# Kernel optimization log

Measured on AMD Instinct MI355X. Metric: run time of the kernel, lower is better.

## Reference

```python
import jax, jax.numpy as jnp
import numpy as np

USER_NUM = 100_000
ITEM_NUM = 50_000
N = USER_NUM + ITEM_NUM          # total nodes in the bipartite graph
HIDDEN = 64
LAYERS = 3
BATCH = 4096
NNZ = 4_800_000                  # ~avg degree 32


def setup_inputs() -> dict:
    key = jax.random.key(0)
    ks = jax.random.split(key, 7)
    emb = jax.random.normal(ks[0], (N, HIDDEN), dtype=jnp.float32) * 0.02
    rows = jax.random.randint(ks[1], (NNZ,), 0, N, dtype=jnp.int32)
    cols = jax.random.randint(ks[2], (NNZ,), 0, N, dtype=jnp.int32)
    # normalized-laplacian-like positive values, scaled ~ 1/avg_degree
    vals = jax.random.uniform(ks[3], (NNZ,), dtype=jnp.float32) * (1.0 / 32.0)
    user = jax.random.randint(ks[4], (BATCH,), 0, USER_NUM, dtype=jnp.int32)
    pos = jax.random.randint(ks[5], (BATCH,), USER_NUM, N, dtype=jnp.int32)
    neg = jax.random.randint(ks[6], (BATCH,), USER_NUM, N, dtype=jnp.int32)
    return {"emb": emb, "vals": vals, "rows": rows, "cols": cols,
            "user": user, "pos": pos, "neg": neg}


def _spmm(rows, cols, vals, x):
    # sparse [N,N] @ dense [N,d] in COO form: gather + scale + segment-sum
    return jax.ops.segment_sum(vals[:, None] * x[cols], rows, num_segments=N)


def reference(emb, vals, rows, cols, user, pos, neg):
    # layer-0 gathers
    user_acc = emb[user]
    pos_acc = emb[pos]
    neg_acc = emb[neg]
    e = emb
    for _ in range(LAYERS):
        e = _spmm(rows, cols, vals, e)
        user_acc = user_acc + e[user]
        pos_acc = pos_acc + e[pos]
        neg_acc = neg_acc + e[neg]
    denom = jnp.float32(LAYERS + 1)
    u = user_acc / denom   # mean over stacked layers
    p = pos_acc / denom
    n = neg_acc / denom
    pos_logits = jnp.einsum('id,id->i', u, p)
    neg_logits = jnp.einsum('id,id->i', u, n)
    # -log(sigmoid(x)) == -log_sigmoid(x) (numerically stable)
    loss = -jax.nn.log_sigmoid(pos_logits - neg_logits)
    return loss.sum()
```

## Files before the change

### kernel.cpp

```cpp
#include <hip/hip_runtime.h>

#define HIDDEN 64
#define PAD 96
#define CHUNK 16384
#define NBMAX 1024
#define E_CAP 9600

typedef unsigned int uint;

__device__ __forceinline__ ushort f2bf(float f) {
    uint u = __float_as_uint(f);
    u = (u + 0x7FFFu + ((u >> 16) & 1u)) >> 16;
    return (ushort)u;
}
__device__ __forceinline__ float bf2f(ushort h) {
    return __uint_as_float(((uint)h) << 16);
}


__global__ void __launch_bounds__(256) k_f2bf(const float4* __restrict__ src,
                                              ushort* __restrict__ dst, int n4) {
    int i = blockIdx.x * blockDim.x + threadIdx.x;
    if (i >= n4) return;
    float4 f = src[i];
    ushort4 o;
    o.x = f2bf(f.x); o.y = f2bf(f.y); o.z = f2bf(f.z); o.w = f2bf(f.w);
    ((ushort4*)dst)[i] = o;
}


__global__ void __launch_bounds__(1024) k_count(const int* __restrict__ rows,
                                                int* __restrict__ partial,
                                                int nnz, int nb) {
    __shared__ int h[NBMAX];
    int t = threadIdx.x;
    for (int i = t; i < nb; i += 1024) h[i] = 0;
    __syncthreads();
    int cb = blockIdx.x * CHUNK;
    #pragma unroll
    for (int j = 0; j < CHUNK / 1024; ++j) {
        int idx = cb + j * 1024 + t;
        if (idx < nnz) atomicAdd(&h[rows[idx] >> 8], 1);
    }
    __syncthreads();
    for (int i = t; i < nb; i += 1024) partial[(size_t)blockIdx.x * nb + i] = h[i];
}

__global__ void __launch_bounds__(1024) k_colscan(const int* __restrict__ partial,
                                                  int* __restrict__ blockoff,
                                                  int* __restrict__ stagecnt,
                                                  int nblk, int nb) {
    __shared__ int s[1024];
    int k = blockIdx.x;
    int t = threadIdx.x;
    int v = (t < nblk) ? partial[(size_t)t * nb + k] : 0;
    s[t] = v;
    __syncthreads();
    for (int d = 1; d < 1024; d <<= 1) {
        int p = (t >= d) ? s[t - d] : 0;
        __syncthreads();
        s[t] += p;
        __syncthreads();
    }
    if (t < nblk) blockoff[(size_t)t * nb + k] = s[t] - v;
    if (t == 1023) stagecnt[k] = s[1023];
}

__global__ void __launch_bounds__(1024) k_bucketscan(const int* __restrict__ stagecnt,
                                                     int* __restrict__ base, int nb) {
    __shared__ int s[1024];
    int t = threadIdx.x;
    int v = (t < nb) ? stagecnt[t] : 0;
    s[t] = v;
    __syncthreads();
    for (int d = 1; d < 1024; d <<= 1) {
        int p = (t >= d) ? s[t - d] : 0;
        __syncthreads();
        s[t] += p;
        __syncthreads();
    }
    if (t < nb) base[t] = s[t] - v;
}

__global__ void __launch_bounds__(1024) k_stage(const int* __restrict__ rows,
                                                const int* __restrict__ cols,
                                                const float* __restrict__ vals,
                                                const int* __restrict__ blockoff,
                                                const int* __restrict__ base,
                                                int2* __restrict__ staged,
                                                int nnz, int nb) {
    __shared__ int cur[NBMAX];
    int t = threadIdx.x;
    for (int i = t; i < nb; i += 1024)
        cur[i] = base[i] + blockoff[(size_t)blockIdx.x * nb + i];
    __syncthreads();
    int cb = blockIdx.x * CHUNK;
    #pragma unroll
    for (int j = 0; j < CHUNK / 1024; ++j) {
        int idx = cb + j * 1024 + t;
        if (idx < nnz) {
            int r = rows[idx];
            int k = r >> 8;
            int slot = atomicAdd(&cur[k], 1);
            staged[slot] = make_int2(cols[idx] | ((r & 255) << 18),
                                     __float_as_int(vals[idx]));
        }
    }
}

__global__ void __launch_bounds__(1024) k_fine(const int2* __restrict__ staged,
                                               const int* __restrict__ base,
                                               const int* __restrict__ stagecnt,
                                               int2* __restrict__ pack,
                                               int* __restrict__ cnt, int n) {
    __shared__ int2 out[E_CAP];
    __shared__ int hist[256], rstart[256], cursor[256], s2[256];
    int k = blockIdx.x;
    int t = threadIdx.x;
    int s0 = base[k];
    int ck = stagecnt[k];
    if (t < 256) hist[t] = 0;
    __syncthreads();
    for (int i = t; i < ck; i += 1024)
        atomicAdd(&hist[((uint)staged[s0 + i].x) >> 18], 1);
    __syncthreads();
    if (t < 256) s2[t] = hist[t];
    __syncthreads();
    for (int d = 1; d < 256; d <<= 1) {
        int p = (t < 256 && t >= d) ? s2[t - d] : 0;
        __syncthreads();
        if (t < 256) s2[t] += p;
        __syncthreads();
    }
    if (t < 256) {
        int rs = s2[t] - hist[t];
        rstart[t] = rs;
        cursor[t] = rs;
        int row = (k << 8) + t;
        if (row < n) cnt[row] = hist[t];
    }
    __syncthreads();
    for (int i = t; i < ck; i += 1024) {
        int2 e = staged[s0 + i];
        int lr = ((uint)e.x) >> 18;
        int slot = atomicAdd(&cursor[lr], 1);
        if (slot < E_CAP) out[slot] = make_int2(e.x & 0x3FFFF, e.y);
    }
    __syncthreads();
    for (int idx = t; idx < 256 * PAD; idx += 1024) {
        int lr = idx / PAD, j = idx - lr * PAD;
        if (j < hist[lr]) {
            int row = (k << 8) + lr;
            pack[(size_t)row * PAD + j] = out[rstart[lr] + j];
        }
    }
}


__device__ __forceinline__ float4 spmm_row4(const int* __restrict__ cnt,
                                            const int2* __restrict__ pack,
                                            const ushort* __restrict__ x,
                                            int row, int lane) {
    int len = cnt[row]; if (len > PAD) len = PAD;
    const int2* base = pack + (size_t)row * PAD;
    int g = (lane & 15) * 4;
    int e = lane >> 4;
    float a0 = 0.f, a1 = 0.f, a2 = 0.f, a3 = 0.f;
    float b0 = 0.f, b1 = 0.f, b2 = 0.f, b3 = 0.f;
    for (int j0 = 0; j0 < len; j0 += 64) {
        int m = len - j0; if (m > 64) m = 64;
        int c = 0; float v = 0.f;
        if (lane < m) {
            int2 cv = base[j0 + lane];
            c = cv.x;
            v = __int_as_float(cv.y);
        }
        int steps = (m + 3) >> 2;
        int s = 0;
        for (; s + 1 < steps; s += 2) {
            int   i0 = 4 * s + e,  i1 = 4 * s + 4 + e;
            int   c0 = __shfl(c, i0); float v0 = __shfl(v, i0);
            int   c1 = __shfl(c, i1); float v1 = __shfl(v, i1);
            ushort4 x0 = *(const ushort4*)(x + (size_t)c0 * HIDDEN + g);
            ushort4 x1 = *(const ushort4*)(x + (size_t)c1 * HIDDEN + g);
            a0 += v0 * bf2f(x0.x); a1 += v0 * bf2f(x0.y);
            a2 += v0 * bf2f(x0.z); a3 += v0 * bf2f(x0.w);
            b0 += v1 * bf2f(x1.x); b1 += v1 * bf2f(x1.y);
            b2 += v1 * bf2f(x1.z); b3 += v1 * bf2f(x1.w);
        }
        if (s < steps) {
            int i0 = 4 * s + e;
            int c0 = __shfl(c, i0); float v0 = __shfl(v, i0);
            ushort4 x0 = *(const ushort4*)(x + (size_t)c0 * HIDDEN + g);
            a0 += v0 * bf2f(x0.x); a1 += v0 * bf2f(x0.y);
            a2 += v0 * bf2f(x0.z); a3 += v0 * bf2f(x0.w);
        }
    }
    a0 += b0; a1 += b1; a2 += b2; a3 += b3;
    a0 += __shfl_xor(a0, 16); a1 += __shfl_xor(a1, 16);
    a2 += __shfl_xor(a2, 16); a3 += __shfl_xor(a3, 16);
    a0 += __shfl_xor(a0, 32); a1 += __shfl_xor(a1, 32);
    a2 += __shfl_xor(a2, 32); a3 += __shfl_xor(a3, 32);
    return make_float4(a0, a1, a2, a3);
}

__global__ void __launch_bounds__(256) k_spmm(const int* __restrict__ cnt,
                                              const int2* __restrict__ pack,
                                              const ushort* __restrict__ x,
                                              ushort* __restrict__ y, int n) {
    int row  = (int)((blockIdx.x * blockDim.x + threadIdx.x) >> 6);
    int lane = threadIdx.x & 63;
    if (row >= n) return;
    float4 a = spmm_row4(cnt, pack, x, row, lane);
    if (lane < 16) {
        ushort4 o;
        o.x = f2bf(a.x); o.y = f2bf(a.y); o.z = f2bf(a.z); o.w = f2bf(a.w);
        *(ushort4*)(y + (size_t)row * HIDDEN + lane * 4) = o;
    }
}

__global__ void __launch_bounds__(256) k_spmm_batch(const int* __restrict__ cnt,
                                                    const int2* __restrict__ pack,
                                                    const ushort* __restrict__ x,
                                                    const int* __restrict__ user,
                                                    const int* __restrict__ pos,
                                                    const int* __restrict__ neg,
                                                    int batch, float* __restrict__ acc) {
    int slot = (int)((blockIdx.x * blockDim.x + threadIdx.x) >> 6);
    int lane = threadIdx.x & 63;
    if (slot >= 3 * batch) return;
    int which = slot / batch, i = slot - which * batch;
    const int* sel = (which == 0) ? user : (which == 1 ? pos : neg);
    float4 a = spmm_row4(cnt, pack, x, sel[i], lane);
    if (lane < 16) {
        float4* p = (float4*)(acc + (size_t)slot * HIDDEN + lane * 4);
        float4 old = *p;
        old.x += a.x; old.y += a.y; old.z += a.z; old.w += a.w;
        *p = old;
    }
}


__global__ void __launch_bounds__(256) k_gather0(const float* __restrict__ e,
                                                 const int* __restrict__ user,
                                                 const int* __restrict__ pos,
                                                 const int* __restrict__ neg,
                                                 int batch, float* __restrict__ acc) {
    int row  = (int)((blockIdx.x * blockDim.x + threadIdx.x) >> 6);
    int lane = threadIdx.x & 63;
    if (row >= 3 * batch) return;
    int which = row / batch, i = row - which * batch;
    const int* sel = (which == 0) ? user : (which == 1 ? pos : neg);
    int s = sel[i];
    acc[(size_t)row * HIDDEN + lane] = e[(size_t)s * HIDDEN + lane];
}

__global__ void __launch_bounds__(256) k_gather_bf(const ushort* __restrict__ e,
                                                   const int* __restrict__ user,
                                                   const int* __restrict__ pos,
                                                   const int* __restrict__ neg,
                                                   int batch, float* __restrict__ acc) {
    int row  = (int)((blockIdx.x * blockDim.x + threadIdx.x) >> 6);
    int lane = threadIdx.x & 63;
    if (row >= 3 * batch) return;
    int which = row / batch, i = row - which * batch;
    const int* sel = (which == 0) ? user : (which == 1 ? pos : neg);
    int s = sel[i];
    acc[(size_t)row * HIDDEN + lane] += bf2f(e[(size_t)s * HIDDEN + lane]);
}


__global__ void __launch_bounds__(256) k_loss(const float* __restrict__ acc, int batch,
                                              float* __restrict__ out) {
    int i    = (int)((blockIdx.x * blockDim.x + threadIdx.x) >> 6);
    int lane = threadIdx.x & 63;
    if (i >= batch) return;
    float u  = acc[(size_t)i * HIDDEN + lane] * 0.25f;
    float p  = acc[(size_t)(i + batch) * HIDDEN + lane] * 0.25f;
    float nn = acc[(size_t)(i + 2 * batch) * HIDDEN + lane] * 0.25f;
    float sp = u * p, sn = u * nn;
    for (int d = 32; d > 0; d >>= 1) {
        sp += __shfl_down(sp, d);
        sn += __shfl_down(sn, d);
    }
    if (lane == 0) {
        float z = sn - sp;
        float loss = fmaxf(z, 0.f) + log1pf(expf(-fabsf(z)));
        atomicAdd(out, loss);
    }
}


extern "C" void kernel_launch(void* const* d_in, const int* in_sizes, int n_in,
                              void* d_out, int out_size, void* d_ws, size_t ws_size,
                              hipStream_t stream) {
    (void)n_in; (void)out_size; (void)ws_size;
    const float* emb  = (const float*)d_in[0];
    const float* vals = (const float*)d_in[1];
    const int*   rows = (const int*)d_in[2];
    const int*   cols = (const int*)d_in[3];
    const int*   user = (const int*)d_in[4];
    const int*   pos  = (const int*)d_in[5];
    const int*   neg  = (const int*)d_in[6];

    const int n     = in_sizes[0] / HIDDEN;
    const int nnz   = in_sizes[1];
    const int batch = in_sizes[4];

    const int nb   = (n + 255) >> 8;
    const int nblk = (nnz + CHUNK - 1) / CHUNK;

    auto align256 = [](size_t x) { return (x + 255) & ~(size_t)255; };
    char* w = (char*)d_ws;
    int*    cnt      = (int*)w;    w += align256(sizeof(int)  * (size_t)n);
    int*    partial  = (int*)w;    w += align256(sizeof(int)  * (size_t)nblk * nb);
    int*    blockoff = (int*)w;    w += align256(sizeof(int)  * (size_t)nblk * nb);
    int*    stagecnt = (int*)w;    w += align256(sizeof(int)  * (size_t)nb);
    int*    base     = (int*)w;    w += align256(sizeof(int)  * (size_t)nb);
    int2*   pack     = (int2*)w;   w += align256(sizeof(int2) * (size_t)n * PAD);
    ushort* emb_bf   = (ushort*)w; w += align256(sizeof(ushort) * (size_t)n * HIDDEN);
    ushort* e0       = (ushort*)w; w += align256(sizeof(ushort) * (size_t)n * HIDDEN);
    ushort* e1       = (ushort*)w; w += align256(sizeof(ushort) * (size_t)n * HIDDEN);
    float*  acc      = (float*)w;  w += align256(sizeof(float)  * (size_t)3 * batch * HIDDEN);

    int2* staged = (int2*)emb_bf;

    float* out = (float*)d_out;

    const int B = 256;
    dim3 blk(B);
    int g_conv  = (n * HIDDEN / 4 + B - 1) / B;
    int g_spmm  = (n + 3) / 4;
    int g_gath  = (3 * batch + 3) / 4;
    int g_loss  = (batch + 3) / 4;

    k_count<<<nblk, 1024, 0, stream>>>(rows, partial, nnz, nb);
    k_colscan<<<nb, 1024, 0, stream>>>(partial, blockoff, stagecnt, nblk, nb);
    k_bucketscan<<<1, 1024, 0, stream>>>(stagecnt, base, nb);
    k_stage<<<nblk, 1024, 0, stream>>>(rows, cols, vals, blockoff, base, staged, nnz, nb);
    k_fine<<<nb, 1024, 0, stream>>>(staged, base, stagecnt, pack, cnt, n);

    k_f2bf<<<g_conv, blk, 0, stream>>>((const float4*)emb, emb_bf, n * HIDDEN / 4);

    hipMemsetAsync(out, 0, sizeof(float), stream);

    k_gather0<<<g_gath, blk, 0, stream>>>(emb, user, pos, neg, batch, acc);
    k_spmm<<<g_spmm, blk, 0, stream>>>(cnt, pack, emb_bf, e0, n);
    k_gather_bf<<<g_gath, blk, 0, stream>>>(e0, user, pos, neg, batch, acc);
    k_spmm<<<g_spmm, blk, 0, stream>>>(cnt, pack, e0, e1, n);
    k_gather_bf<<<g_gath, blk, 0, stream>>>(e1, user, pos, neg, batch, acc);
    k_spmm_batch<<<g_gath, blk, 0, stream>>>(cnt, pack, e1, user, pos, neg, batch, acc);

    k_loss<<<g_loss, blk, 0, stream>>>(acc, batch, out);
}
```

Baseline: 359.8 us.

## Replace multi-pass counting sort with single-pass atomic-cursor bucketing into fixed-capacity slots

Replaces the count, column-scan, bucket-scan and stage kernels with one kernel. Each block histograms its chunk in shared memory, reserves space per bucket with a global atomic cursor, sorts locally in LDS, then writes runs contiguously into fixed-capacity per-bucket regions. This removes several launches and the extra full read of rows. The cost is nondeterministic edge order within a bucket and a hard per-bucket capacity, so edges beyond CAP are silently dropped.

```diff
diff --git a/kernel.cpp b/kernel.cpp
--- a/kernel.cpp
+++ b/kernel.cpp
@@ -2,9 +2,9 @@
 
 #define HIDDEN 64
 #define PAD 96
-#define CHUNK 16384
-#define NBMAX 1024
-#define E_CAP 9600
+#define CHUNK 8192
+#define NBMAX 640
+#define CAP 9600
 
 typedef unsigned int uint;
 
@@ -29,96 +29,123 @@
 }
 
 
-__global__ void __launch_bounds__(1024) k_count(const int* __restrict__ rows,
-                                                int* __restrict__ partial,
-                                                int nnz, int nb) {
-    __shared__ int h[NBMAX];
-    int t = threadIdx.x;
-    for (int i = t; i < nb; i += 1024) h[i] = 0;
-    __syncthreads();
+__global__ void __launch_bounds__(512) k_stage(const int* __restrict__ rows,
+                                               const int* __restrict__ cols,
+                                               const float* __restrict__ vals,
+                                               int* __restrict__ cursor,
+                                               int2* __restrict__ staged,
+                                               int nnz, int nb) {
+    __shared__ int  hS[NBMAX];
+    __shared__ int  lsS[NBMAX];
+    __shared__ int  gsS[NBMAX];
+    __shared__ int  lcS[NBMAX];
+    __shared__ int  ps[512];
+    __shared__ int2 stg[CHUNK];
+
+    int t  = threadIdx.x;
     int cb = blockIdx.x * CHUNK;
+
+    for (int k = t; k < nb; k += 512) hS[k] = 0;
+    __syncthreads();
+
+    int4 ra[4];
     #pragma unroll
-    for (int j = 0; j < CHUNK / 1024; ++j) {
-        int idx = cb + j * 1024 + t;
-        if (idx < nnz) atomicAdd(&h[rows[idx] >> 8], 1);
-    }
-    __syncthreads();
-    for (int i = t; i < nb; i += 1024) partial[(size_t)blockIdx.x * nb + i] = h[i];
-}
-
-__global__ void __launch_bounds__(1024) k_colscan(const int* __restrict__ partial,
-                                                  int* __restrict__ blockoff,
-                                                  int* __restrict__ stagecnt,
-                                                  int nblk, int nb) {
-    __shared__ int s[1024];
-    int k = blockIdx.x;
-    int t = threadIdx.x;
-    int v = (t < nblk) ? partial[(size_t)t * nb + k] : 0;
-    s[t] = v;
-    __syncthreads();
-    for (int d = 1; d < 1024; d <<= 1) {
-        int p = (t >= d) ? s[t - d] : 0;
+    for (int j = 0; j < 4; ++j) {
+        int idx = cb + j * 2048 + t * 4;
+        int4 r4;
+        if (idx + 3 < nnz) {
+            r4 = *(const int4*)(rows + idx);
+        } else {
+            r4.x = (idx     < nnz) ? rows[idx]     : -1;
+            r4.y = (idx + 1 < nnz) ? rows[idx + 1] : -1;
+            r4.z = (idx + 2 < nnz) ? rows[idx + 2] : -1;
+            r4.w = (idx + 3 < nnz) ? rows[idx + 3] : -1;
+        }
+        ra[j] = r4;
+        if (r4.x >= 0) atomicAdd(&hS[r4.x >> 8], 1);
+        if (r4.y >= 0) atomicAdd(&hS[r4.y >> 8], 1);
+        if (r4.z >= 0) atomicAdd(&hS[r4.z >> 8], 1);
+        if (r4.w >= 0) atomicAdd(&hS[r4.w >> 8], 1);
+    }
+    __syncthreads();
+
+    int k0 = 2 * t, k1 = 2 * t + 1;
+    int c0 = (k0 < nb) ? hS[k0] : 0;
+    int c1 = (k1 < nb) ? hS[k1] : 0;
+    ps[t] = c0 + c1;
+    __syncthreads();
+    for (int d = 1; d < 512; d <<= 1) {
+        int p = (t >= d) ? ps[t - d] : 0;
         __syncthreads();
-        s[t] += p;
+        ps[t] += p;
         __syncthreads();
     }
-    if (t < nblk) blockoff[(size_t)t * nb + k] = s[t] - v;
-    if (t == 1023) stagecnt[k] = s[1023];
-}
-
-__global__ void __launch_bounds__(1024) k_bucketscan(const int* __restrict__ stagecnt,
-                                                     int* __restrict__ base, int nb) {
-    __shared__ int s[1024];
-    int t = threadIdx.x;
-    int v = (t < nb) ? stagecnt[t] : 0;
-    s[t] = v;
-    __syncthreads();
-    for (int d = 1; d < 1024; d <<= 1) {
-        int p = (t >= d) ? s[t - d] : 0;
-        __syncthreads();
-        s[t] += p;
-        __syncthreads();
-    }
-    if (t < nb) base[t] = s[t] - v;
-}
-
-__global__ void __launch_bounds__(1024) k_stage(const int* __restrict__ rows,
-                                                const int* __restrict__ cols,
-                                                const float* __restrict__ vals,
-                                                const int* __restrict__ blockoff,
-                                                const int* __restrict__ base,
-                                                int2* __restrict__ staged,
-                                                int nnz, int nb) {
-    __shared__ int cur[NBMAX];
-    int t = threadIdx.x;
-    for (int i = t; i < nb; i += 1024)
-        cur[i] = base[i] + blockoff[(size_t)blockIdx.x * nb + i];
-    __syncthreads();
-    int cb = blockIdx.x * CHUNK;
+    int excl = ps[t] - (c0 + c1);
+    if (k0 < nb) {
+        lsS[k0] = excl;
+        gsS[k0] = atomicAdd(&cursor[k0], c0);
+    }
+    if (k1 < nb) {
+        lsS[k1] = excl + c0;
+        gsS[k1] = atomicAdd(&cursor[k1], c1);
+    }
+    __syncthreads();
+    for (int k = t; k < nb; k += 512) lcS[k] = lsS[k];
+    __syncthreads();
+
     #pragma unroll
-    for (int j = 0; j < CHUNK / 1024; ++j) {
-        int idx = cb + j * 1024 + t;
-        if (idx < nnz) {
-            int r = rows[idx];
-            int k = r >> 8;
-            int slot = atomicAdd(&cur[k], 1);
-            staged[slot] = make_int2(cols[idx] | ((r & 255) << 18),
-                                     __float_as_int(vals[idx]));
-        }
+    for (int j = 0; j < 4; ++j) {
+        int idx = cb + j * 2048 + t * 4;
+        int4 r4 = ra[j];
+        int4 c4; float4 v4;
+        if (idx + 3 < nnz) {
+            c4 = *(const int4*)(cols + idx);
+            v4 = *(const float4*)(vals + idx);
+        } else {
+            c4.x = (idx     < nnz) ? cols[idx]     : 0;
+            c4.y = (idx + 1 < nnz) ? cols[idx + 1] : 0;
+            c4.z = (idx + 2 < nnz) ? cols[idx + 2] : 0;
+            c4.w = (idx + 3 < nnz) ? cols[idx + 3] : 0;
+            v4.x = (idx     < nnz) ? vals[idx]     : 0.f;
+            v4.y = (idx + 1 < nnz) ? vals[idx + 1] : 0.f;
+            v4.z = (idx + 2 < nnz) ? vals[idx + 2] : 0.f;
+            v4.w = (idx + 3 < nnz) ? vals[idx + 3] : 0.f;
+        }
+        if (r4.x >= 0) { int s = atomicAdd(&lcS[r4.x >> 8], 1);
+            stg[s] = make_int2(c4.x | ((r4.x & 255) << 18), __float_as_int(v4.x)); }
+        if (r4.y >= 0) { int s = atomicAdd(&lcS[r4.y >> 8], 1);
+            stg[s] = make_int2(c4.y | ((r4.y & 255) << 18), __float_as_int(v4.y)); }
+        if (r4.z >= 0) { int s = atomicAdd(&lcS[r4.z >> 8], 1);
+            stg[s] = make_int2(c4.z | ((r4.z & 255) << 18), __float_as_int(v4.z)); }
+        if (r4.w >= 0) { int s = atomicAdd(&lcS[r4.w >> 8], 1);
+            stg[s] = make_int2(c4.w | ((r4.w & 255) << 18), __float_as_int(v4.w)); }
+    }
+    __syncthreads();
+
+    int m_total = nnz - cb; if (m_total > CHUNK) m_total = CHUNK;
+    for (int i = t; i < m_total; i += 512) {
+        int2 e = stg[i];
+        int lo = 0, hi = nb - 1;
+        while (lo < hi) {
+            int mid = (lo + hi + 1) >> 1;
+            if (lsS[mid] <= i) lo = mid; else hi = mid - 1;
+        }
+        int k = lo;
+        int pos = gsS[k] + (i - lsS[k]);
+        if (pos < CAP) staged[(size_t)k * CAP + pos] = e;
     }
 }
 
 __global__ void __launch_bounds__(1024) k_fine(const int2* __restrict__ staged,
-                                               const int* __restrict__ base,
                                                const int* __restrict__ stagecnt,
                                                int2* __restrict__ pack,
                                                int* __restrict__ cnt, int n) {
-    __shared__ int2 out[E_CAP];
+    __shared__ int2 out[CAP];
     __shared__ int hist[256], rstart[256], cursor[256], s2[256];
     int k = blockIdx.x;
     int t = threadIdx.x;
-    int s0 = base[k];
-    int ck = stagecnt[k];
+    size_t s0 = (size_t)k * CAP;
+    int ck = stagecnt[k]; if (ck > CAP) ck = CAP;
     if (t < 256) hist[t] = 0;
     __syncthreads();
     for (int i = t; i < ck; i += 1024)
@@ -144,7 +171,7 @@
         int2 e = staged[s0 + i];
         int lr = ((uint)e.x) >> 18;
         int slot = atomicAdd(&cursor[lr], 1);
-        if (slot < E_CAP) out[slot] = make_int2(e.x & 0x3FFFF, e.y);
+        if (slot < CAP) out[slot] = make_int2(e.x & 0x3FFFF, e.y);
     }
     __syncthreads();
     for (int idx = t; idx < 256 * PAD; idx += 1024) {
@@ -312,18 +339,18 @@
 
     auto align256 = [](size_t x) { return (x + 255) & ~(size_t)255; };
     char* w = (char*)d_ws;
-    int*    cnt      = (int*)w;    w += align256(sizeof(int)  * (size_t)n);
-    int*    partial  = (int*)w;    w += align256(sizeof(int)  * (size_t)nblk * nb);
-    int*    blockoff = (int*)w;    w += align256(sizeof(int)  * (size_t)nblk * nb);
-    int*    stagecnt = (int*)w;    w += align256(sizeof(int)  * (size_t)nb);
-    int*    base     = (int*)w;    w += align256(sizeof(int)  * (size_t)nb);
-    int2*   pack     = (int2*)w;   w += align256(sizeof(int2) * (size_t)n * PAD);
-    ushort* emb_bf   = (ushort*)w; w += align256(sizeof(ushort) * (size_t)n * HIDDEN);
-    ushort* e0       = (ushort*)w; w += align256(sizeof(ushort) * (size_t)n * HIDDEN);
-    ushort* e1       = (ushort*)w; w += align256(sizeof(ushort) * (size_t)n * HIDDEN);
-    float*  acc      = (float*)w;  w += align256(sizeof(float)  * (size_t)3 * batch * HIDDEN);
+    int*    cnt    = (int*)w;    w += align256(sizeof(int)  * (size_t)n);
+    int*    cursor = (int*)w;    w += align256(sizeof(int)  * (size_t)NBMAX);
+    int2*   pack   = (int2*)w;   w += align256(sizeof(int2) * (size_t)n * PAD);
+    ushort* emb_bf = (ushort*)w; w += align256(sizeof(ushort) * (size_t)n * HIDDEN);
+    ushort* e0     = (ushort*)w; w += align256(sizeof(ushort) * (size_t)n * HIDDEN);
+    ushort* e1     = (ushort*)w; w += align256(sizeof(ushort) * (size_t)n * HIDDEN);
+    float*  acc    = (float*)w;  w += align256(sizeof(float)  * (size_t)3 * batch * HIDDEN);
+    int2*   stg_x  = (int2*)w;   w += align256(sizeof(int2) * ((size_t)nb * CAP > 3u * n * HIDDEN ?
+                                               (size_t)nb * CAP - 3u * n * HIDDEN : 0));
 
     int2* staged = (int2*)emb_bf;
+    (void)stg_x;
 
     float* out = (float*)d_out;
 
@@ -334,11 +361,9 @@
     int g_gath  = (3 * batch + 3) / 4;
     int g_loss  = (batch + 3) / 4;
 
-    k_count<<<nblk, 1024, 0, stream>>>(rows, partial, nnz, nb);
-    k_colscan<<<nb, 1024, 0, stream>>>(partial, blockoff, stagecnt, nblk, nb);
-    k_bucketscan<<<1, 1024, 0, stream>>>(stagecnt, base, nb);
-    k_stage<<<nblk, 1024, 0, stream>>>(rows, cols, vals, blockoff, base, staged, nnz, nb);
-    k_fine<<<nb, 1024, 0, stream>>>(staged, base, stagecnt, pack, cnt, n);
+    hipMemsetAsync(cursor, 0, sizeof(int) * (size_t)NBMAX, stream);
+    k_stage<<<nblk, 512, 0, stream>>>(rows, cols, vals, cursor, staged, nnz, nb);
+    k_fine<<<nb, 1024, 0, stream>>>(staged, cursor, pack, cnt, n);
 
     k_f2bf<<<g_conv, blk, 0, stream>>>((const float4*)emb, emb_bf, n * HIDDEN / 4);
 
```

Result: faster. 348.4 us (-3.2%).
